# Kernel tuning notes

Measured on AMD Instinct MI355X. Metric: run time of the kernel, lower is better.

## Reference

```python
import jax, jax.numpy as jnp
import numpy as np

KSIZE = 21
SCALE = 4

def _conv1x1(h, w, b):
    # h: (B, Ci, H, W), w: (Co, Ci), b: (Co,)
    return jnp.einsum('oi,bihw->bohw', w, h) + b[None, :, None, None]

def setup_inputs() -> dict:
    key = jax.random.key(0)
    ks = jax.random.split(key, 8)
    B, C, H, W = 16, 3, 256, 256
    in_nc, nf, nb, K2 = 64, 64, 8, KSIZE * KSIZE
    Hl, Wl = H // SCALE, W // SCALE
    wscale = 0.1
    return {
        'x': jax.random.normal(ks[0], (B, C, H, W), jnp.float32),
        'z': jax.random.normal(ks[1], (B, in_nc, Hl, Wl), jnp.float32),
        'w_in': wscale * jax.random.normal(ks[2], (nf, in_nc), jnp.float32),
        'b_in': jnp.zeros((nf,), jnp.float32),
        'res_w1': wscale * jax.random.normal(ks[3], (nb, nf, nf), jnp.float32),
        'res_b1': jnp.zeros((nb, nf), jnp.float32),
        'res_w2': wscale * jax.random.normal(ks[4], (nb, nf, nf), jnp.float32),
        'res_b2': jnp.zeros((nb, nf), jnp.float32),
        'w_out': wscale * jax.random.normal(ks[5], (K2, nf), jnp.float32),
        'b_out': jnp.zeros((K2,), jnp.float32),
    }

def reference(x, z, w_in, b_in, res_w1, res_b1, res_w2, res_b2, w_out, b_out):
    B, C, H, W = x.shape
    Hl, Wl = z.shape[2], z.shape[3]
    K2 = KSIZE * KSIZE
    pad = KSIZE // 2

    # --- kernel prediction trunk (all 1x1 convs) ---
    h = _conv1x1(z, w_in, b_in)
    for i in range(res_w1.shape[0]):  # fixed n_layers loop
        r = _conv1x1(h, res_w1[i], res_b1[i])
        r = _conv1x1(jax.nn.relu(r), res_w2[i], res_b2[i])
        h = h + r
    logits = _conv1x1(h, w_out, b_out)            # (B, K2, Hl, Wl)
    kernel = jax.nn.softmax(logits, axis=1)       # softmax over kernel taps

    # --- reflection pad + unfold (im2col) with stride=scale ---
    xp = jnp.pad(x, ((0, 0), (0, 0), (pad, pad), (pad, pad)), mode='reflect')
    xr = xp.reshape(B * C, 1, H + 2 * pad, W + 2 * pad)
    patches = jax.lax.conv_general_dilated_patches(
        xr, filter_shape=(KSIZE, KSIZE), window_strides=(SCALE, SCALE),
        padding='VALID', dimension_numbers=('NCHW', 'OIHW', 'NCHW'))
    patches = patches.reshape(B, C, K2, Hl, Wl)   # (B, C, K2, Hl, Wl)

    # --- per-pixel spatially-varying kernel apply ---
    out = (patches * kernel[:, None]).sum(axis=2)  # (B, C, Hl, Wl)
    return out, kernel
```

## Files before the change

### kernel.cpp

```cpp
#include <hip/hip_runtime.h>
#include <math.h>

#define KS 21
#define K2 441
#define NB 8
#define PPI 4096
#define NPIX 65536
#define STR 72
#define XW 276
#define BPX 256
#define NTH 1024
#define XROWS 33
#define XRS 2208

typedef unsigned short u16;
typedef unsigned int u32;
typedef short short8v __attribute__((ext_vector_type(8)));
typedef float f32x4 __attribute__((ext_vector_type(4)));
typedef float f32x16 __attribute__((ext_vector_type(16)));
typedef u32 u32x2v __attribute__((ext_vector_type(2)));

#define WOUT_OFF 69632
#define BOUT_BYTE 196608

#define LDS_HBUF  0
#define LDS_XS    36864
#define LDS_BSH   109728
#define LDS_SBUF  111520
#define LDS_OBUF  113568
#define LDS_TOTAL 119712

#define BAR_LDS()                                                   \
    do {                                                            \
        asm volatile("s_waitcnt lgkmcnt(0)" ::: "memory");          \
        __builtin_amdgcn_s_barrier();                               \
        __builtin_amdgcn_sched_barrier(0);                          \
    } while (0)

__device__ __forceinline__ u16 f2bf(float x)
{
    union { float f; u32 u; } c; c.f = x;
    u32 r = c.u + 0x7FFF + ((c.u >> 16) & 1);
    return (u16)(r >> 16);
}
__device__ __forceinline__ float bflo(u32 w)
{ union { u32 u; float f; } c; c.u = w << 16; return c.f; }
__device__ __forceinline__ float bfhi(u32 w)
{ union { u32 u; float f; } c; c.u = w & 0xffff0000u; return c.f; }

__device__ __forceinline__ int xcd_swz(int i)
{
    return ((i & 7) << 5) | (i >> 3);
}

__device__ __forceinline__ u32 xs_off(int row, int col)
{
    u32 off = (u32)row * XRS + (u32)col * 8;
    return off ^ ((((u32)col >> 4) & 3) << 3);
}

__global__ void prep_kernel(const float* __restrict__ w_in,
                            const float* __restrict__ rw1,
                            const float* __restrict__ rw2,
                            const float* __restrict__ w_out,
                            const float* __restrict__ b_out,
                            u16* __restrict__ wsu, float* __restrict__ bout)
{
    int idx = blockIdx.x * 256 + threadIdx.x;
    if (idx < 69632) {
        int u = idx & 4095;
        int j = u & 7, lane = (u >> 3) & 63, frag = (u >> 9) & 7;
        int kk = frag >> 2, nt = frag & 3, layer = idx >> 12;
        int i = kk * 32 + (lane >> 4) * 8 + j;
        int o = nt * 16 + (lane & 15);
        const float* src;
        if (layer == 0) src = w_in;
        else if (layer & 1) src = rw1 + ((layer - 1) >> 1) * 4096;
        else src = rw2 + ((layer - 2) >> 1) * 4096;
        wsu[idx] = f2bf(src[o * 64 + i]);
    } else if (idx < 69632 + 28672) {
        int u = idx - 69632;
        int j = u & 7, lane = (u >> 3) & 63, t6 = u >> 9;
        int t = t6 % 14, kk = t6 / 14;
        int tap = t * 32 + (lane & 31);
        int i = kk * 16 + (lane >> 5) * 8 + j;
        wsu[idx] = f2bf((tap < K2) ? w_out[tap * 64 + i] : 0.f);
    } else if (idx < 69632 + 28672 + 448) {
        int tap = idx - (69632 + 28672);
        bout[tap] = (tap < K2) ? b_out[tap] : -100.f;
    }
}

__device__ __forceinline__ int reflect256(int v)
{
    v = (v < 0) ? -v : v;
    return (v > 255) ? (510 - v) : v;
}

template <int MODE>
__device__ __forceinline__ void do_layer(u16* hb, const u16* __restrict__ wb,
                                         const float* __restrict__ bias,
                                         float* hreg, int aoff, int wbase,
                                         int c, int g, int lane)
{
    short8v a0 = *(const short8v*)(hb + aoff);
    short8v a1 = *(const short8v*)(hb + aoff + 32);
#pragma unroll
    for (int nt = 0; nt < 4; ++nt) {
        f32x4 acc = {};
        short8v b0 = *(const short8v*)(wb + ((nt)     * 64 + lane) * 8);
        short8v b1 = *(const short8v*)(wb + ((4 + nt) * 64 + lane) * 8);
        acc = __builtin_amdgcn_mfma_f32_16x16x32_bf16(a0, b0, acc, 0, 0, 0);
        acc = __builtin_amdgcn_mfma_f32_16x16x32_bf16(a1, b1, acc, 0, 0, 0);
        const float bv = bias[nt * 16 + c];
#pragma unroll
        for (int r = 0; r < 4; ++r) {
            float v = acc[r] + bv;
            if (MODE == 1) v = fmaxf(v, 0.f);
            if (MODE == 2) { v += hreg[nt * 4 + r]; hreg[nt * 4 + r] = v; }
            if (MODE == 0) hreg[nt * 4 + r] = v;
            hb[(wbase + g * 4 + r) * STR + nt * 16 + c] = f2bf(v);
        }
    }
}

__launch_bounds__(NTH, 1)
__global__ void trunk_kernel(const float* __restrict__ z,
                             const float* __restrict__ x,
                             const float* __restrict__ b_in,
                             const float* __restrict__ rb1,
                             const float* __restrict__ rb2,
                             const u16* __restrict__ wsu,
                             const float* __restrict__ bout,
                             float* __restrict__ out,
                             float* __restrict__ kout)
{
    extern __shared__ __align__(16) char smem[];
    u16*   hbuf = (u16*)(smem + LDS_HBUF);
    char*  xsb  = smem + LDS_XS;
    float* bsh  = (float*)(smem + LDS_BSH);
    float* sbuf = (float*)(smem + LDS_SBUF);
    float* obuf = (float*)(smem + LDS_OBUF);

    const int tid = threadIdx.x, lane = tid & 63, wave = tid >> 6;
    const int pix0 = xcd_swz(blockIdx.x) * BPX;
    const int b = pix0 >> 12, rem0 = pix0 & 4095;
    const int hl0 = rem0 >> 6;

    {
        const int p = tid & 255, i0 = (tid >> 8) * 16;
        const float* zp = z + ((size_t)b * 64 + i0) * PPI + rem0 + p;
        u32* dst = (u32*)hbuf + p * (STR / 2) + i0 / 2;
#pragma unroll
        for (int i = 0; i < 16; i += 2) {
            float v0 = zp[(size_t)i * PPI];
            float v1 = zp[(size_t)(i + 1) * PPI];
            dst[i / 2] = (u32)f2bf(v0) | ((u32)f2bf(v1) << 16);
        }
    }
    for (int u = tid; u < XROWS * XW; u += NTH) {
        int rr = u / XW, c = u - rr * XW;
        int row = reflect256(hl0 * 4 + rr - 10);
        int xcol = reflect256(c - 10);
        const float* xp = x + (size_t)b * 3 * 65536 + row * 256 + xcol;
        u32 w0 = (u32)f2bf(xp[0]) | ((u32)f2bf(xp[65536]) << 16);
        u32 w1 = (u32)f2bf(xp[2 * 65536]);
        u32x2v wv; wv[0] = w0; wv[1] = w1;
        *(u32x2v*)(xsb + xs_off(rr, c)) = wv;
    }
    if (tid < 448) bsh[tid] = bout[tid];
    BAR_LDS();

    const int c16 = lane & 15, g4 = lane >> 4;
    const int wbase = wave * 16;
    const int aoff = (wbase + c16) * STR + g4 * 8;
    float hreg[16];

    do_layer<0>(hbuf, wsu, b_in, hreg, aoff, wbase, c16, g4, lane);
#pragma unroll 1
    for (int l = 0; l < NB; ++l) {
        do_layer<1>(hbuf, wsu + (size_t)(1 + 2 * l) * 4096, rb1 + l * 64,
                    hreg, aoff, wbase, c16, g4, lane);
        do_layer<2>(hbuf, wsu + (size_t)(2 + 2 * l) * 4096, rb2 + l * 64,
                    hreg, aoff, wbase, c16, g4, lane);
    }
    BAR_LDS();

    const int c32 = lane & 31, hi2 = lane >> 5;
    const int wavepx = (wave >> 1) * 32;
    const int tbase = (wave & 1) * 7;

    short8v bh[4];
#pragma unroll
    for (int kk = 0; kk < 4; ++kk)
        bh[kk] = *(const short8v*)(hbuf + (wavepx + c32) * STR + kk * 16 + hi2 * 8);

    float ssum = 0.f;
    u32 epack[56];
    const u16* wob = wsu + WOUT_OFF;
#pragma unroll
    for (int ti = 0; ti < 7; ++ti) {
        const int t = tbase + ti;
        f32x16 acc = {};
#pragma unroll
        for (int kk = 0; kk < 4; ++kk) {
            short8v aw = *(const short8v*)(wob + ((kk * 14 + t) * 64 + lane) * 8);
            acc = __builtin_amdgcn_mfma_f32_32x32x16_bf16(aw, bh[kk], acc, 0, 0, 0);
        }
#pragma unroll
        for (int rr = 0; rr < 8; ++rr) {
            const int r0 = 2 * rr;
            const int tap0 = t * 32 + (r0 & 3) + 8 * (r0 >> 2) + 4 * hi2;
            float e0 = __expf(acc[r0] + bsh[tap0]);
            float e1 = __expf(acc[r0 + 1] + bsh[tap0 + 1]);
            ssum += e0 + e1;
            epack[ti * 8 + rr] = (u32)f2bf(e0) | ((u32)f2bf(e1) << 16);
        }
    }
    ssum += __shfl_xor(ssum, 32);
    if (lane < 32) sbuf[wave * 32 + lane] = ssum;
    BAR_LDS();
    const float inv_s = 1.f / (ssum + sbuf[(wave ^ 1) * 32 + c32]);

    const int pxl = wavepx + c32;
    const int wl = pxl & 63, hlr = pxl >> 6;
    const int xcb4 = wl * 4;
    float* kbase = kout + (size_t)b * K2 * PPI + rem0 + pxl;
    float oacc0 = 0.f, oacc1 = 0.f, oacc2 = 0.f;

#pragma unroll
    for (int ti = 0; ti < 7; ++ti) {
        const int t = tbase + ti;
        int tap = t * 32 + 4 * hi2;
        int ky = tap / KS;
        int kx = tap - ky * KS;
#pragma unroll
        for (int rr = 0; rr < 8; ++rr) {
            const u32 ep = epack[ti * 8 + rr];
            float p0 = bflo(ep) * inv_s;
            float p1 = bfhi(ep) * inv_s;
            if (tap < K2) {
                kbase[(size_t)tap * PPI] = p0;
                u32x2v wv = *(const u32x2v*)(xsb + xs_off(hlr * 4 + ky, xcb4 + kx));
                oacc0 = fmaf(p0, bflo(wv[0]), oacc0);
                oacc1 = fmaf(p0, bfhi(wv[0]), oacc1);
                oacc2 = fmaf(p0, bflo(wv[1]), oacc2);
            }
            tap += 1; kx += 1; if (kx >= KS) { kx -= KS; ky += 1; }
            if (tap < K2) {
                kbase[(size_t)tap * PPI] = p1;
                u32x2v wv = *(const u32x2v*)(xsb + xs_off(hlr * 4 + ky, xcb4 + kx));
                oacc0 = fmaf(p1, bflo(wv[0]), oacc0);
                oacc1 = fmaf(p1, bfhi(wv[0]), oacc1);
                oacc2 = fmaf(p1, bflo(wv[1]), oacc2);
            }
            const int d = (rr & 1) ? 5 : 1;
            tap += d; kx += d; if (kx >= KS) { kx -= KS; ky += 1; }
        }
    }

    oacc0 += __shfl_xor(oacc0, 32);
    oacc1 += __shfl_xor(oacc1, 32);
    oacc2 += __shfl_xor(oacc2, 32);
    if (lane < 32) {
        obuf[(wave * 3 + 0) * 32 + lane] = oacc0;
        obuf[(wave * 3 + 1) * 32 + lane] = oacc1;
        obuf[(wave * 3 + 2) * 32 + lane] = oacc2;
    }
    BAR_LDS();
    if ((wave & 1) == 0 && lane < 32) {
        const int o = rem0 + wavepx + lane;
#pragma unroll
        for (int cch = 0; cch < 3; ++cch) {
            float v = obuf[(wave * 3 + cch) * 32 + lane] +
                      obuf[((wave + 1) * 3 + cch) * 32 + lane];
            out[((size_t)b * 3 + cch) * PPI + o] = v;
        }
    }
}

extern "C" void kernel_launch(void* const* d_in, const int* in_sizes, int n_in,
                              void* d_out, int out_size, void* d_ws, size_t ws_size,
                              hipStream_t stream)
{
    const float* x     = (const float*)d_in[0];
    const float* z     = (const float*)d_in[1];
    const float* w_in  = (const float*)d_in[2];
    const float* b_in  = (const float*)d_in[3];
    const float* rw1   = (const float*)d_in[4];
    const float* rb1   = (const float*)d_in[5];
    const float* rw2   = (const float*)d_in[6];
    const float* rb2   = (const float*)d_in[7];
    const float* w_out = (const float*)d_in[8];
    const float* b_out = (const float*)d_in[9];

    float* out  = (float*)d_out;
    float* kout = out + (size_t)16 * 3 * PPI;
    u16*   wsu  = (u16*)d_ws;
    float* bout = (float*)((char*)d_ws + BOUT_BYTE);

    (void)hipFuncSetAttribute((const void*)trunk_kernel,
                              hipFuncAttributeMaxDynamicSharedMemorySize,
                              LDS_TOTAL);

    prep_kernel<<<(69632 + 28672 + 448 + 255) / 256, 256, 0, stream>>>(
        w_in, rw1, rw2, w_out, b_out, wsu, bout);

    trunk_kernel<<<NPIX / BPX, NTH, LDS_TOTAL, stream>>>(
        z, x, b_in, rb1, rb2, wsu, bout, out, kout);
}
```

Measured before the change: 74.68 us.

## Pre-pad x to a global bf16 buffer and use small 64-pixel trunk blocks

Adds a separate pad kernel that writes a reflection-padded, channel-interleaved bf16 copy of x into workspace memory. A new trunk_small kernel (256 threads, 64 pixels per block, static LDS) reads the patch values straight from that global buffer, so it no longer stages a 33-row x tile in LDS. The intent is higher occupancy, with many small blocks per CU instead of one 1024-thread block, and no duplicated per-block padding work. The costs are an extra kernel launch plus a global write and read of the padded image, and patch reads now go to global or cache memory instead of LDS. The old path is kept as a fallback when the workspace is too small.

```diff
diff --git a/kernel.cpp b/kernel.cpp
--- a/kernel.cpp
+++ b/kernel.cpp
@@ -8,10 +8,10 @@
 #define NPIX 65536
 #define STR 72
 #define XW 276
-#define BPX 256
-#define NTH 1024
-#define XROWS 33
-#define XRS 2208
+#define XDIM 276
+#define XRS (XDIM * 8)
+#define XIMG ((size_t)XDIM * XDIM * 8)
+#define XPAD_OFF 200704
 
 typedef unsigned short u16;
 typedef unsigned int u32;
@@ -29,6 +29,7 @@
 #define LDS_SBUF  111520
 #define LDS_OBUF  113568
 #define LDS_TOTAL 119712
+#define XROWS 33
 
 #define BAR_LDS()                                                   \
     do {                                                            \
@@ -48,7 +49,17 @@
 __device__ __forceinline__ float bfhi(u32 w)
 { union { u32 u; float f; } c; c.u = w & 0xffff0000u; return c.f; }
 
-__device__ __forceinline__ int xcd_swz(int i)
+__device__ __forceinline__ int reflect256(int v)
+{
+    v = (v < 0) ? -v : v;
+    return (v > 255) ? (510 - v) : v;
+}
+
+__device__ __forceinline__ int xcd_swz1024(int i)
+{
+    return ((i & 7) << 7) | (i >> 3);
+}
+__device__ __forceinline__ int xcd_swz256(int i)
 {
     return ((i & 7) << 5) | (i >> 3);
 }
@@ -91,10 +102,19 @@
     }
 }
 
-__device__ __forceinline__ int reflect256(int v)
-{
-    v = (v < 0) ? -v : v;
-    return (v > 255) ? (510 - v) : v;
+__global__ void pad_kernel(const float* __restrict__ x, char* __restrict__ xpad)
+{
+    int idx = blockIdx.x * 256 + threadIdx.x;
+    if (idx >= 16 * XDIM * XDIM) return;
+    int b = idx / (XDIM * XDIM);
+    int r = idx - b * (XDIM * XDIM);
+    int row = r / XDIM, col = r - row * XDIM;
+    int sr = reflect256(row - 10), sc = reflect256(col - 10);
+    const float* xp = x + (size_t)b * 3 * 65536 + sr * 256 + sc;
+    u32 w0 = (u32)f2bf(xp[0]) | ((u32)f2bf(xp[65536]) << 16);
+    u32 w1 = (u32)f2bf(xp[2 * 65536]);
+    u32x2v wv; wv[0] = w0; wv[1] = w1;
+    *(u32x2v*)(xpad + (size_t)b * XIMG + (size_t)row * XRS + col * 8) = wv;
 }
 
 template <int MODE>
@@ -124,7 +144,148 @@
     }
 }
 
-__launch_bounds__(NTH, 1)
+__launch_bounds__(256, 8)
+__global__ void trunk_small(const float* __restrict__ z,
+                            const char* __restrict__ xpad,
+                            const float* __restrict__ b_in,
+                            const float* __restrict__ rb1,
+                            const float* __restrict__ rb2,
+                            const u16* __restrict__ wsu,
+                            const float* __restrict__ bout,
+                            float* __restrict__ out,
+                            float* __restrict__ kout)
+{
+    __shared__ __align__(16) u16 hbuf[64 * STR];
+    __shared__ float bsh[448];
+    __shared__ float sbuf[4][32];
+    __shared__ float obuf[4][3][32];
+
+    const int tid = threadIdx.x, lane = tid & 63, wave = tid >> 6;
+    const int pix0 = xcd_swz1024(blockIdx.x) * 64;
+    const int b = pix0 >> 12, rem0 = pix0 & 4095;
+    const int hl = rem0 >> 6;
+
+    {
+        const int p = tid & 63, i0 = (tid >> 6) * 16;
+        const float* zp = z + ((size_t)b * 64 + i0) * PPI + rem0 + p;
+        u32* dst = (u32*)hbuf + p * (STR / 2) + i0 / 2;
+#pragma unroll
+        for (int i = 0; i < 16; i += 2) {
+            float v0 = zp[(size_t)i * PPI];
+            float v1 = zp[(size_t)(i + 1) * PPI];
+            dst[i / 2] = (u32)f2bf(v0) | ((u32)f2bf(v1) << 16);
+        }
+    }
+    for (int u = tid; u < 448; u += 256) bsh[u] = bout[u];
+    BAR_LDS();
+
+    const int c16 = lane & 15, g4 = lane >> 4;
+    const int wbase = wave * 16;
+    const int aoff = (wbase + c16) * STR + g4 * 8;
+    float hreg[16];
+
+    do_layer<0>(hbuf, wsu, b_in, hreg, aoff, wbase, c16, g4, lane);
+#pragma unroll 1
+    for (int l = 0; l < NB; ++l) {
+        do_layer<1>(hbuf, wsu + (size_t)(1 + 2 * l) * 4096, rb1 + l * 64,
+                    hreg, aoff, wbase, c16, g4, lane);
+        do_layer<2>(hbuf, wsu + (size_t)(2 + 2 * l) * 4096, rb2 + l * 64,
+                    hreg, aoff, wbase, c16, g4, lane);
+    }
+    BAR_LDS();
+
+    const int c32 = lane & 31, hi2 = lane >> 5;
+    const int wavepx = (wave >> 1) * 32;
+    const int tbase = (wave & 1) * 7;
+
+    short8v bh[4];
+#pragma unroll
+    for (int kk = 0; kk < 4; ++kk)
+        bh[kk] = *(const short8v*)(hbuf + (wavepx + c32) * STR + kk * 16 + hi2 * 8);
+
+    float ssum = 0.f;
+    u32 epack[56];
+    const u16* wob = wsu + WOUT_OFF;
+#pragma unroll
+    for (int ti = 0; ti < 7; ++ti) {
+        const int t = tbase + ti;
+        f32x16 acc = {};
+#pragma unroll
+        for (int kk = 0; kk < 4; ++kk) {
+            short8v aw = *(const short8v*)(wob + ((kk * 14 + t) * 64 + lane) * 8);
+            acc = __builtin_amdgcn_mfma_f32_32x32x16_bf16(aw, bh[kk], acc, 0, 0, 0);
+        }
+#pragma unroll
+        for (int rr = 0; rr < 8; ++rr) {
+            const int r0 = 2 * rr;
+            const int tap0 = t * 32 + (r0 & 3) + 8 * (r0 >> 2) + 4 * hi2;
+            float e0 = __expf(acc[r0] + bsh[tap0]);
+            float e1 = __expf(acc[r0 + 1] + bsh[tap0 + 1]);
+            ssum += e0 + e1;
+            epack[ti * 8 + rr] = (u32)f2bf(e0) | ((u32)f2bf(e1) << 16);
+        }
+    }
+    ssum += __shfl_xor(ssum, 32);
+    if (lane < 32) sbuf[wave][lane] = ssum;
+    BAR_LDS();
+    const float inv_s = 1.f / (ssum + sbuf[wave ^ 1][c32]);
+
+    const int pxl = wavepx + c32;
+    float* kbase = kout + (size_t)b * K2 * PPI + rem0 + pxl;
+    const char* xb = xpad + (size_t)b * XIMG + (size_t)(hl * 4) * XRS + pxl * 32;
+    float oacc0 = 0.f, oacc1 = 0.f, oacc2 = 0.f;
+
+#pragma unroll
+    for (int ti = 0; ti < 7; ++ti) {
+        const int t = tbase + ti;
+        int tap = t * 32 + 4 * hi2;
+        int ky = tap / KS;
+        int kx = tap - ky * KS;
+#pragma unroll
+        for (int rr = 0; rr < 8; ++rr) {
+            const u32 ep = epack[ti * 8 + rr];
+            float p0 = bflo(ep) * inv_s;
+            float p1 = bfhi(ep) * inv_s;
+            if (tap < K2) {
+                kbase[(size_t)tap * PPI] = p0;
+                u32x2v wv = *(const u32x2v*)(xb + ky * XRS + kx * 8);
+                oacc0 = fmaf(p0, bflo(wv[0]), oacc0);
+                oacc1 = fmaf(p0, bfhi(wv[0]), oacc1);
+                oacc2 = fmaf(p0, bflo(wv[1]), oacc2);
+            }
+            tap += 1; kx += 1; if (kx >= KS) { kx -= KS; ky += 1; }
+            if (tap < K2) {
+                kbase[(size_t)tap * PPI] = p1;
+                u32x2v wv = *(const u32x2v*)(xb + ky * XRS + kx * 8);
+                oacc0 = fmaf(p1, bflo(wv[0]), oacc0);
+                oacc1 = fmaf(p1, bfhi(wv[0]), oacc1);
+                oacc2 = fmaf(p1, bflo(wv[1]), oacc2);
+            }
+            const int d = (rr & 1) ? 5 : 1;
+            tap += d; kx += d; if (kx >= KS) { kx -= KS; ky += 1; }
+        }
+    }
+
+    oacc0 += __shfl_xor(oacc0, 32);
+    oacc1 += __shfl_xor(oacc1, 32);
+    oacc2 += __shfl_xor(oacc2, 32);
+    if (lane < 32) {
+        obuf[wave][0][lane] = oacc0;
+        obuf[wave][1][lane] = oacc1;
+        obuf[wave][2][lane] = oacc2;
+    }
+    BAR_LDS();
+    if ((wave & 1) == 0 && lane < 32) {
+        const int o = rem0 + wavepx + lane;
+#pragma unroll
+        for (int cch = 0; cch < 3; ++cch) {
+            float v = obuf[wave][cch][lane] + obuf[wave + 1][cch][lane];
+            out[((size_t)b * 3 + cch) * PPI + o] = v;
+        }
+    }
+}
+
+__launch_bounds__(1024, 1)
 __global__ void trunk_kernel(const float* __restrict__ z,
                              const float* __restrict__ x,
                              const float* __restrict__ b_in,
@@ -143,7 +304,7 @@
     float* obuf = (float*)(smem + LDS_OBUF);
 
     const int tid = threadIdx.x, lane = tid & 63, wave = tid >> 6;
-    const int pix0 = xcd_swz(blockIdx.x) * BPX;
+    const int pix0 = xcd_swz256(blockIdx.x) * 256;
     const int b = pix0 >> 12, rem0 = pix0 & 4095;
     const int hl0 = rem0 >> 6;
 
@@ -158,7 +319,7 @@
             dst[i / 2] = (u32)f2bf(v0) | ((u32)f2bf(v1) << 16);
         }
     }
-    for (int u = tid; u < XROWS * XW; u += NTH) {
+    for (int u = tid; u < XROWS * XW; u += 1024) {
         int rr = u / XW, c = u - rr * XW;
         int row = reflect256(hl0 * 4 + rr - 10);
         int xcol = reflect256(c - 10);
@@ -299,13 +460,20 @@
     u16*   wsu  = (u16*)d_ws;
     float* bout = (float*)((char*)d_ws + BOUT_BYTE);
 
-    (void)hipFuncSetAttribute((const void*)trunk_kernel,
-                              hipFuncAttributeMaxDynamicSharedMemorySize,
-                              LDS_TOTAL);
-
     prep_kernel<<<(69632 + 28672 + 448 + 255) / 256, 256, 0, stream>>>(
         w_in, rw1, rw2, w_out, b_out, wsu, bout);
 
-    trunk_kernel<<<NPIX / BPX, NTH, LDS_TOTAL, stream>>>(
-        z, x, b_in, rb1, rb2, wsu, bout, out, kout);
-}
+    const size_t need = (size_t)XPAD_OFF + 16 * XIMG;
+    if (ws_size >= need) {
+        char* xpad = (char*)d_ws + XPAD_OFF;
+        pad_kernel<<<(16 * XDIM * XDIM + 255) / 256, 256, 0, stream>>>(x, xpad);
+        trunk_small<<<NPIX / 64, 256, 0, stream>>>(
+            z, xpad, b_in, rb1, rb2, wsu, bout, out, kout);
+    } else {
+        (void)hipFuncSetAttribute((const void*)trunk_kernel,
+                                  hipFuncAttributeMaxDynamicSharedMemorySize,
+                                  LDS_TOTAL);
+        trunk_kernel<<<NPIX / 256, 1024, LDS_TOTAL, stream>>>(
+            z, x, b_in, rb1, rb2, wsu, bout, out, kout);
+    }
+}
```

Result: slower. 192.4 us (+157.7%).
